# Optimization experiments

Measured on AMD Instinct MI355X. Metric: run time of the kernel, lower is better.

Reference implementation:

```python
import jax, jax.numpy as jnp
import numpy as np

WEIGHT_BITS = 8
INPUT_BITS = 8


def fake_quant(t, bits):
    """Per-tensor symmetric absmax fake quantization with straight-through estimator."""
    qmax = 2.0 ** (bits - 1) - 1.0  # e.g. 127 for 8 bits
    scale = jnp.maximum(jnp.max(jnp.abs(t)), 1e-8) / qmax
    q = jnp.round(t / scale) * scale
    return t + jax.lax.stop_gradient(q - t)


def setup_inputs() -> dict:
    key = jax.random.key(0)
    k0, k1, k2, k3 = jax.random.split(key, 4)
    d, f, n = 4096, 11008, 4096
    s_in = 1.0 / np.sqrt(d)
    s_ff = 1.0 / np.sqrt(f)
    return {
        "x": jax.random.normal(k0, (n, d), jnp.float32),
        "w1": jax.random.normal(k1, (f, d), jnp.float32) * s_in,  # fc1: embed -> ffn
        "w3": jax.random.normal(k2, (f, d), jnp.float32) * s_in,  # fc3: gate proj
        "w2": jax.random.normal(k3, (d, f), jnp.float32) * s_ff,  # fc2: ffn -> embed
    }


def reference(x, w1, w3, w2):
    # quantized fc3 -> silu gate
    xq = fake_quant(x, INPUT_BITS)
    gate = jax.nn.silu(jnp.einsum('nd,fd->nf', xq, fake_quant(w3, WEIGHT_BITS)))
    # quantized fc1, multiplied by gate (GLU)
    h = jnp.einsum('nd,fd->nf', xq, fake_quant(w1, WEIGHT_BITS)) * gate
    # subln=False -> no ffn_layernorm; dropout=0 (eval)
    hq = fake_quant(h, INPUT_BITS)
    out = jnp.einsum('nf,df->nd', hq, fake_quant(w2, WEIGHT_BITS))
    return out
```

## Files before the change

kernel.cpp:

```cpp
#include <hip/hip_runtime.h>
#include <hip/hip_bf16.h>

typedef __attribute__((ext_vector_type(4))) int int4v;

#define MFMA_I8(a, b, c) __builtin_amdgcn_mfma_i32_16x16x64_i8((a), (b), (c), 0, 0, 0)
#define GLDS16(g, l)                                                                        \
  __builtin_amdgcn_global_load_lds((const __attribute__((address_space(1))) void*)(g),      \
                                   (__attribute__((address_space(3))) void*)(l), 16, 0, 0)
#define SBAR() __builtin_amdgcn_s_barrier()
#define SCHED0() __builtin_amdgcn_sched_barrier(0)

static constexpr int NTOK = 4096;
static constexpr int DDIM = 4096;
static constexpr int FDIM = 11008;


__device__ __forceinline__ float wave_max64(float m) {
#pragma unroll
  for (int o = 32; o > 0; o >>= 1) m = fmaxf(m, __shfl_xor(m, o));
  return m;
}

__global__ void zero_slots(unsigned* s) {
  if (threadIdx.x < 16) s[threadIdx.x] = 0u;
}

__device__ __forceinline__ void absmax_body(const float* __restrict__ p, int n4,
                                            unsigned* __restrict__ slot) {
  float m = 0.f;
  const int stride = gridDim.x * blockDim.x;
  for (int i = blockIdx.x * blockDim.x + threadIdx.x; i < n4; i += stride) {
    float4 v = reinterpret_cast<const float4*>(p)[i];
    m = fmaxf(fmaxf(fabsf(v.x), fabsf(v.y)), fmaxf(fmaxf(fabsf(v.z), fabsf(v.w)), m));
  }
  m = wave_max64(m);
  __shared__ float wm[4];
  const int lane = threadIdx.x & 63, w = threadIdx.x >> 6;
  if (lane == 0) wm[w] = m;
  __syncthreads();
  if (threadIdx.x == 0) {
    m = fmaxf(fmaxf(wm[0], wm[1]), fmaxf(wm[2], wm[3]));
    atomicMax(slot, __float_as_uint(m));
  }
}

__global__ void absmax4(const float* x, const float* w1, const float* w3, const float* w2,
                        unsigned* slots, int n4x, int n4w) {
  const int seg = blockIdx.y;
  const float* p = (seg == 0) ? x : (seg == 1) ? w1 : (seg == 2) ? w3 : w2;
  absmax_body(p, seg == 0 ? n4x : n4w, slots + seg);
}

__device__ __forceinline__ void quant_body(const float* __restrict__ in,
                                           unsigned* __restrict__ out, int n4,
                                           const unsigned* __restrict__ slot) {
  const float s = fmaxf(__uint_as_float(*slot), 1e-8f) / 127.0f;
  const int stride = gridDim.x * blockDim.x;
  for (int i = blockIdx.x * blockDim.x + threadIdx.x; i < n4; i += stride) {
    float4 v = reinterpret_cast<const float4*>(in)[i];
    const int q0 = (int)rintf(v.x / s), q1 = (int)rintf(v.y / s);
    const int q2 = (int)rintf(v.z / s), q3 = (int)rintf(v.w / s);
    out[i] = (unsigned)(q0 & 255) | ((unsigned)(q1 & 255) << 8) |
             ((unsigned)(q2 & 255) << 16) | ((unsigned)(q3 & 255) << 24);
  }
}

__global__ void quant4(const float* x, const float* w1, const float* w3, const float* w2,
                       unsigned* qx, unsigned* qw1, unsigned* qw3, unsigned* qw2,
                       const unsigned* slots, int n4x, int n4w) {
  const int seg = blockIdx.y;
  const float* p = (seg == 0) ? x : (seg == 1) ? w1 : (seg == 2) ? w3 : w2;
  unsigned* o = (seg == 0) ? qx : (seg == 1) ? qw1 : (seg == 2) ? qw3 : qw2;
  quant_body(p, o, seg == 0 ? n4x : n4w, slots + seg);
}

__global__ void quant_kernel(const float* __restrict__ in, unsigned* __restrict__ out,
                             int n4, const unsigned* __restrict__ slot) {
  quant_body(in, out, n4, slot);
}

__global__ __launch_bounds__(512, 2) void gemm_glu(
    const signed char* __restrict__ Aq, const signed char* __restrict__ B3q,
    const signed char* __restrict__ B1q, float* __restrict__ H,
    const unsigned* __restrict__ slots, unsigned* __restrict__ hslot) {
  constexpr int K = DDIM;
  __shared__ char lds[163840];

  const int t = threadIdx.x;
  const int l = t & 63;
  const int w = t >> 6;

  const int gx = gridDim.x, gy = gridDim.y;
  const int nwg = gx * gy;
  const int i0 = blockIdx.y * gx + blockIdx.x;
  const int cid = (i0 & 7) * (nwg >> 3) + (i0 >> 3);
  const int rowA0 = (cid % gy) << 7;
  const int colB0 = (cid / gy) << 8;

  const int rlA = t >> 3;
  const int glA = (t & 7) ^ (rlA & 7);
  const signed char* aP = Aq + (size_t)(rowA0 + rlA) * K + glA * 16;
  const size_t r64 = (size_t)64 * K;
  const int stW = w * 1024;

  const int rlB = l >> 3;
  const int glB = (l & 7) ^ rlB;
  const signed char* b3P = B3q + (size_t)(colB0 + w * 32 + rlB) * K + glB * 16;
  const signed char* b1P = B1q + (size_t)(colB0 + w * 32 + rlB) * K + glB * 16;
  const size_t r8 = (size_t)8 * K;
  const int bBase3 = 16384 + w * 4096;
  const int bBase1 = 49152 + w * 4096;

#define STAGE_A(KO, BUF)                            \
  do {                                              \
    GLDS16(aP + (KO), &lds[(BUF) + stW]);           \
    GLDS16(aP + r64 + (KO), &lds[(BUF) + 8192 + stW]); \
  } while (0)

#define STAGE_B(KO, BUF)                                           \
  do {                                                             \
    GLDS16(b3P + (KO), &lds[(BUF) + bBase3]);                      \
    GLDS16(b3P + r8 + (KO), &lds[(BUF) + bBase3 + 1024]);          \
    GLDS16(b3P + 2 * r8 + (KO), &lds[(BUF) + bBase3 + 2048]);      \
    GLDS16(b3P + 3 * r8 + (KO), &lds[(BUF) + bBase3 + 3072]);      \
    GLDS16(b1P + (KO), &lds[(BUF) + bBase1]);                      \
    GLDS16(b1P + r8 + (KO), &lds[(BUF) + bBase1 + 1024]);          \
    GLDS16(b1P + 2 * r8 + (KO), &lds[(BUF) + bBase1 + 2048]);      \
    GLDS16(b1P + 3 * r8 + (KO), &lds[(BUF) + bBase1 + 3072]);      \
  } while (0)

#define LDSF(BASE, R, G)                                                      \
  (*reinterpret_cast<const int4v*>(                                           \
      &lds[(BASE) + (R)*128 + (((G) ^ ((R)&7)) << 4)]))

  int4v acc3[8][2], acc1[8][2];
#pragma unroll
  for (int m = 0; m < 8; ++m)
#pragma unroll
    for (int n = 0; n < 2; ++n) {
      acc3[m][n] = (int4v){0, 0, 0, 0};
      acc1[m][n] = (int4v){0, 0, 0, 0};
    }

  const int NT = K >> 7;
  const int lr = l & 15;
  const int cr = l >> 4;

  STAGE_A(0, 0);
  STAGE_B(0, 0);

  for (int kt = 0; kt < NT; ++kt) {
    const int rb = (kt & 1) * 81920;
    const bool haveNext = (kt + 1 < NT);

    SCHED0();
    asm volatile("s_waitcnt vmcnt(8)" ::: "memory");
    SBAR();
    SCHED0();

    if (haveNext) {
      const size_t kO = (size_t)(kt + 1) * 128;
      STAGE_A(kO, rb ^ 81920);
      STAGE_B(kO, rb ^ 81920);
    }

    int4v a[8];
#pragma unroll
    for (int m = 0; m < 8; ++m) a[m] = LDSF(rb, m * 16 + lr, cr);

    if (haveNext) {
      asm volatile("s_waitcnt vmcnt(10)" ::: "memory");
    } else {
      asm volatile("s_waitcnt vmcnt(0)" ::: "memory");
    }
    SCHED0();

    int4v b3f[2][2], b1f[2][2];
#pragma unroll
    for (int n = 0; n < 2; ++n) {
      const int R = n * 16 + lr;
      b3f[0][n] = LDSF(rb + bBase3, R, cr);
      b3f[1][n] = LDSF(rb + bBase3, R, 4 + cr);
      b1f[0][n] = LDSF(rb + bBase1, R, cr);
      b1f[1][n] = LDSF(rb + bBase1, R, 4 + cr);
    }

    __builtin_amdgcn_s_setprio(1);
#pragma unroll
    for (int m = 0; m < 8; ++m)
#pragma unroll
      for (int n = 0; n < 2; ++n) {
        acc3[m][n] = MFMA_I8(a[m], b3f[0][n], acc3[m][n]);
        acc1[m][n] = MFMA_I8(a[m], b1f[0][n], acc1[m][n]);
      }
    __builtin_amdgcn_s_setprio(0);

#pragma unroll
    for (int m = 0; m < 8; ++m) a[m] = LDSF(rb, m * 16 + lr, 4 + cr);
    __builtin_amdgcn_s_setprio(1);
#pragma unroll
    for (int m = 0; m < 8; ++m)
#pragma unroll
      for (int n = 0; n < 2; ++n) {
        acc3[m][n] = MFMA_I8(a[m], b3f[1][n], acc3[m][n]);
        acc1[m][n] = MFMA_I8(a[m], b1f[1][n], acc1[m][n]);
      }
    __builtin_amdgcn_s_setprio(0);
  }

  const float sx = fmaxf(__uint_as_float(slots[0]), 1e-8f) / 127.0f;
  const float sw1 = fmaxf(__uint_as_float(slots[1]), 1e-8f) / 127.0f;
  const float sw3 = fmaxf(__uint_as_float(slots[2]), 1e-8f) / 127.0f;
  const float s3 = sx * sw3, s1 = sx * sw1;
  const int crow0 = rowA0 + ((l >> 4) << 2);
  const int ccol0 = colB0 + w * 32 + lr;
  float hmax = 0.f;
#pragma unroll
  for (int m = 0; m < 8; ++m)
#pragma unroll
    for (int n = 0; n < 2; ++n)
#pragma unroll
      for (int j = 0; j < 4; ++j) {
        const int row = crow0 + m * 16 + j;
        const int col = ccol0 + n * 16;
        const float g = (float)acc3[m][n][j] * s3;
        const float gate = g / (1.f + expf(-g));
        const float h = (float)acc1[m][n][j] * s1 * gate;
        H[(size_t)row * FDIM + col] = h;
        hmax = fmaxf(hmax, fabsf(h));
      }
  hmax = wave_max64(hmax);
  if (l == 0) atomicMax(hslot, __float_as_uint(hmax));
#undef STAGE_A
#undef STAGE_B
#undef LDSF
}

__global__ __launch_bounds__(512, 2) void gemm_down(
    const signed char* __restrict__ Aq, const signed char* __restrict__ Bq,
    float* __restrict__ C, const unsigned* __restrict__ slots, int sA, int sB,
    int K, int ldc) {
  __shared__ char lds[131072];

  const int t = threadIdx.x;
  const int l = t & 63;
  const int w = t >> 6;
  const int wm = w >> 2;
  const int wn = w & 3;

  const int gx = gridDim.x, gy = gridDim.y;
  const int nwg = gx * gy;
  const int i0 = blockIdx.y * gx + blockIdx.x;
  const int cid = (i0 & 7) * (nwg >> 3) + (i0 >> 3);
  const int rowA0 = (cid % gy) << 8;
  const int colB0 = (cid / gy) << 8;

  const int rl = t >> 3;
  const int gl = (t & 7) ^ (rl & 7);
  const signed char* aP = Aq + (size_t)(rowA0 + rl) * K + gl * 16;
  const signed char* bP = Bq + (size_t)(colB0 + rl) * K + gl * 16;
  const size_t r64 = (size_t)64 * K;
  const int stW = w * 1024;

#define STAGE8(KO, BASE)                                             \
  do {                                                               \
    GLDS16(aP + (KO), &lds[(BASE) + stW]);                           \
    GLDS16(aP + r64 + (KO), &lds[(BASE) + 8192 + stW]);              \
    GLDS16(aP + 2 * r64 + (KO), &lds[(BASE) + 16384 + stW]);         \
    GLDS16(aP + 3 * r64 + (KO), &lds[(BASE) + 24576 + stW]);         \
    GLDS16(bP + (KO), &lds[(BASE) + 32768 + stW]);                   \
    GLDS16(bP + r64 + (KO), &lds[(BASE) + 40960 + stW]);             \
    GLDS16(bP + 2 * r64 + (KO), &lds[(BASE) + 49152 + stW]);         \
    GLDS16(bP + 3 * r64 + (KO), &lds[(BASE) + 57344 + stW]);         \
  } while (0)

#define LDSF(BASE, ROW, G)                                                    \
  (*reinterpret_cast<const int4v*>(                                           \
      &lds[(BASE) + (ROW)*128 + (((G) ^ ((ROW)&7)) << 4)]))

  int4v acc[8][4];
#pragma unroll
  for (int m = 0; m < 8; ++m)
#pragma unroll
    for (int n = 0; n < 4; ++n) acc[m][n] = (int4v){0, 0, 0, 0};

  const int NT = K >> 7;
  const int arow = wm * 128 + (l & 15);
  const int brow = wn * 64 + (l & 15);
  const int cr = l >> 4;

  STAGE8(0, 0);

  for (int kt = 0; kt < NT; ++kt) {
    const int rb = (kt & 1) * 65536;
    SCHED0();
    asm volatile("s_waitcnt vmcnt(0)" ::: "memory");
    SBAR();
    SCHED0();

    if (kt + 1 < NT) STAGE8((size_t)(kt + 1) * 128, rb ^ 65536);

#pragma unroll
    for (int kk = 0; kk < 2; ++kk) {
      int4v a[8], b[4];
#pragma unroll
      for (int m = 0; m < 8; ++m) a[m] = LDSF(rb, arow + m * 16, kk * 4 + cr);
#pragma unroll
      for (int n = 0; n < 4; ++n) b[n] = LDSF(rb + 32768, brow + n * 16, kk * 4 + cr);
      __builtin_amdgcn_s_setprio(1);
#pragma unroll
      for (int m = 0; m < 8; ++m)
#pragma unroll
        for (int n = 0; n < 4; ++n) acc[m][n] = MFMA_I8(a[m], b[n], acc[m][n]);
      __builtin_amdgcn_s_setprio(0);
    }
  }

  const float sa = fmaxf(__uint_as_float(slots[sA]), 1e-8f) / 127.0f;
  const float sb2 = fmaxf(__uint_as_float(slots[sB]), 1e-8f) / 127.0f;
  const float s = sa * sb2;
  const int crow0 = rowA0 + wm * 128 + ((l >> 4) << 2);
  const int ccol0 = colB0 + wn * 64 + (l & 15);
#pragma unroll
  for (int m = 0; m < 8; ++m)
#pragma unroll
    for (int n = 0; n < 4; ++n)
#pragma unroll
      for (int j = 0; j < 4; ++j) {
        const int row = crow0 + m * 16 + j;
        const int col = ccol0 + n * 16;
        C[(size_t)row * ldc + col] = (float)acc[m][n][j] * s;
      }
#undef STAGE8
#undef LDSF
}


extern "C" void kernel_launch(void* const* d_in, const int* in_sizes, int n_in,
                              void* d_out, int out_size, void* d_ws, size_t ws_size,
                              hipStream_t stream) {
  const float* x = (const float*)d_in[0];
  const float* w1 = (const float*)d_in[1];
  const float* w3 = (const float*)d_in[2];
  const float* w2 = (const float*)d_in[3];
  float* out = (float*)d_out;
  char* ws = (char*)d_ws;

  unsigned* slots = (unsigned*)ws;
  size_t off = 256;
  signed char* qx = (signed char*)(ws + off);
  off += (size_t)NTOK * DDIM;
  signed char* qw3 = (signed char*)(ws + off);
  off += (size_t)FDIM * DDIM;
  signed char* qw1 = (signed char*)(ws + off);
  off += (size_t)FDIM * DDIM;
  signed char* qw2 = (signed char*)(ws + off);
  off += (size_t)FDIM * DDIM;
  float* H = (float*)(ws + off);
  off += (size_t)NTOK * FDIM * 4;
  signed char* qh = (signed char*)(ws + off);
  off += (size_t)NTOK * FDIM;

  const int n4x = NTOK * DDIM / 4;
  const int n4w = FDIM * DDIM / 4;
  const int n4h = NTOK * FDIM / 4;

  zero_slots<<<1, 64, 0, stream>>>(slots);
  absmax4<<<dim3(512, 4), 256, 0, stream>>>(x, w1, w3, w2, slots, n4x, n4w);
  quant4<<<dim3(512, 4), 256, 0, stream>>>(x, w1, w3, w2, (unsigned*)qx, (unsigned*)qw1,
                                           (unsigned*)qw3, (unsigned*)qw2, slots, n4x, n4w);

  const dim3 gGlu(FDIM / 256, NTOK / 128);
  gemm_glu<<<gGlu, 512, 0, stream>>>(qx, qw3, qw1, H, slots, slots + 4);
  quant_kernel<<<2048, 256, 0, stream>>>(H, (unsigned*)qh, n4h, slots + 4);
  const dim3 gDn(DDIM / 256, NTOK / 256);
  gemm_down<<<gDn, 512, 0, stream>>>(qh, qw2, out, slots, 4, 3, FDIM, DDIM);
}
```

Measured before the change: 893.0 us.

## Pre-swizzle GLU weights into MFMA fragment order and load B directly to registers

The quantization pass now writes w1 and w3 in a fragment-major layout that matches the MFMA B-operand order for each lane. The GLU GEMM loads those fragments straight from global memory into registers, double-buffered two k-tiles ahead, instead of staging B through LDS. Only A goes through LDS, so LDS use drops from 160KB to 32KB. In exchange, B loads are no longer shared across waves through LDS and rely on global/L2 bandwidth and latency hiding in registers. The quant launch grid is also enlarged.

Result: slower. 1.516 ms (+69.7%).

```diff
diff --git a/kernel.cpp b/kernel.cpp
--- a/kernel.cpp
+++ b/kernel.cpp
@@ -3,6 +3,8 @@
 
 typedef __attribute__((ext_vector_type(4))) int int4v;
 
+#define MFMA_I8(a, b, c) __builtin_amdgcn_mfma_i32_32x32x16_i8
+#undef MFMA_I8
 #define MFMA_I8(a, b, c) __builtin_amdgcn_mfma_i32_16x16x64_i8((a), (b), (c), 0, 0, 0)
 #define GLDS16(g, l)                                                                        \
   __builtin_amdgcn_global_load_lds((const __attribute__((address_space(1))) void*)(g),      \
@@ -65,13 +67,43 @@
   }
 }
 
+__device__ __forceinline__ void quantW_frag_body(const float* __restrict__ in,
+                                                 int4v* __restrict__ out,
+                                                 const unsigned* __restrict__ slot) {
+  const float s = fmaxf(__uint_as_float(*slot), 1e-8f) / 127.0f;
+  const int total = FDIM * (DDIM / 16);
+  const int stride = gridDim.x * blockDim.x;
+  for (int u = blockIdx.x * blockDim.x + threadIdx.x; u < total; u += stride) {
+    const int block = u >> 8;
+    const int sidx = u & 255;
+    const int fi = sidx >> 6;
+    const int l = sidx & 63;
+    const int p = block >> 5;
+    const int kt = block & 31;
+    const int f = p * 32 + (fi & 1) * 16 + (l & 15);
+    const int k0 = kt * 128 + (fi >> 1) * 64 + (l >> 4) * 16;
+    const float4* src = reinterpret_cast<const float4*>(in + (size_t)f * DDIM + k0);
+    unsigned r[4];
+#pragma unroll
+    for (int j = 0; j < 4; ++j) {
+      float4 v = src[j];
+      const int q0 = (int)rintf(v.x / s), q1 = (int)rintf(v.y / s);
+      const int q2 = (int)rintf(v.z / s), q3 = (int)rintf(v.w / s);
+      r[j] = (unsigned)(q0 & 255) | ((unsigned)(q1 & 255) << 8) |
+             ((unsigned)(q2 & 255) << 16) | ((unsigned)(q3 & 255) << 24);
+    }
+    out[u] = (int4v){(int)r[0], (int)r[1], (int)r[2], (int)r[3]};
+  }
+}
+
 __global__ void quant4(const float* x, const float* w1, const float* w3, const float* w2,
                        unsigned* qx, unsigned* qw1, unsigned* qw3, unsigned* qw2,
                        const unsigned* slots, int n4x, int n4w) {
   const int seg = blockIdx.y;
-  const float* p = (seg == 0) ? x : (seg == 1) ? w1 : (seg == 2) ? w3 : w2;
-  unsigned* o = (seg == 0) ? qx : (seg == 1) ? qw1 : (seg == 2) ? qw3 : qw2;
-  quant_body(p, o, seg == 0 ? n4x : n4w, slots + seg);
+  if (seg == 0) quant_body(x, qx, n4x, slots + 0);
+  else if (seg == 1) quantW_frag_body(w1, (int4v*)qw1, slots + 1);
+  else if (seg == 2) quantW_frag_body(w3, (int4v*)qw3, slots + 2);
+  else quant_body(w2, qw2, n4w, slots + 3);
 }
 
 __global__ void quant_kernel(const float* __restrict__ in, unsigned* __restrict__ out,
@@ -80,11 +112,12 @@
 }
 
 __global__ __launch_bounds__(512, 2) void gemm_glu(
-    const signed char* __restrict__ Aq, const signed char* __restrict__ B3q,
-    const signed char* __restrict__ B1q, float* __restrict__ H,
+    const signed char* __restrict__ Aq, const signed char* __restrict__ B3f,
+    const signed char* __restrict__ B1f, float* __restrict__ H,
     const unsigned* __restrict__ slots, unsigned* __restrict__ hslot) {
   constexpr int K = DDIM;
-  __shared__ char lds[163840];
+  constexpr int NT = K >> 7;
+  __shared__ char lds[32768];
 
   const int t = threadIdx.x;
   const int l = t & 63;
@@ -103,30 +136,29 @@
   const size_t r64 = (size_t)64 * K;
   const int stW = w * 1024;
 
-  const int rlB = l >> 3;
-  const int glB = (l & 7) ^ rlB;
-  const signed char* b3P = B3q + (size_t)(colB0 + w * 32 + rlB) * K + glB * 16;
-  const signed char* b1P = B1q + (size_t)(colB0 + w * 32 + rlB) * K + glB * 16;
-  const size_t r8 = (size_t)8 * K;
-  const int bBase3 = 16384 + w * 4096;
-  const int bBase1 = 49152 + w * 4096;
-
-#define STAGE_A(KO, BUF)                            \
-  do {                                              \
-    GLDS16(aP + (KO), &lds[(BUF) + stW]);           \
-    GLDS16(aP + r64 + (KO), &lds[(BUF) + 8192 + stW]); \
+  const int p0 = (colB0 >> 5) + w;
+  const signed char* w3b = B3f + (size_t)p0 * 32 * 4096 + l * 16;
+  const signed char* w1b = B1f + (size_t)p0 * 32 * 4096 + l * 16;
+
+#define STAGE_A(KT, BUF)                                  \
+  do {                                                    \
+    const size_t kO_ = (size_t)(KT) * 128;                \
+    GLDS16(aP + kO_, &lds[(BUF) + stW]);                  \
+    GLDS16(aP + r64 + kO_, &lds[(BUF) + 8192 + stW]);     \
   } while (0)
 
-#define STAGE_B(KO, BUF)                                           \
-  do {                                                             \
-    GLDS16(b3P + (KO), &lds[(BUF) + bBase3]);                      \
-    GLDS16(b3P + r8 + (KO), &lds[(BUF) + bBase3 + 1024]);          \
-    GLDS16(b3P + 2 * r8 + (KO), &lds[(BUF) + bBase3 + 2048]);      \
-    GLDS16(b3P + 3 * r8 + (KO), &lds[(BUF) + bBase3 + 3072]);      \
-    GLDS16(b1P + (KO), &lds[(BUF) + bBase1]);                      \
-    GLDS16(b1P + r8 + (KO), &lds[(BUF) + bBase1 + 1024]);          \
-    GLDS16(b1P + 2 * r8 + (KO), &lds[(BUF) + bBase1 + 2048]);      \
-    GLDS16(b1P + 3 * r8 + (KO), &lds[(BUF) + bBase1 + 3072]);      \
+#define LOADB(KT, B3A, B1A)                                      \
+  do {                                                           \
+    const signed char* p3_ = w3b + (size_t)(KT)*4096;            \
+    const signed char* p1_ = w1b + (size_t)(KT)*4096;            \
+    B3A[0][0] = *(const int4v*)(p3_);                            \
+    B3A[0][1] = *(const int4v*)(p3_ + 1024);                     \
+    B3A[1][0] = *(const int4v*)(p3_ + 2048);                     \
+    B3A[1][1] = *(const int4v*)(p3_ + 3072);                     \
+    B1A[0][0] = *(const int4v*)(p1_);                            \
+    B1A[0][1] = *(const int4v*)(p1_ + 1024);                     \
+    B1A[1][0] = *(const int4v*)(p1_ + 2048);                     \
+    B1A[1][1] = *(const int4v*)(p1_ + 3072);                     \
   } while (0)
 
 #define LDSF(BASE, R, G)                                                      \
@@ -142,70 +174,54 @@
       acc1[m][n] = (int4v){0, 0, 0, 0};
     }
 
-  const int NT = K >> 7;
   const int lr = l & 15;
   const int cr = l >> 4;
 
+  int4v bc3[2][2], bc1[2][2], bn3[2][2], bn1[2][2];
+
   STAGE_A(0, 0);
-  STAGE_B(0, 0);
-
-  for (int kt = 0; kt < NT; ++kt) {
-    const int rb = (kt & 1) * 81920;
-    const bool haveNext = (kt + 1 < NT);
-
-    SCHED0();
-    asm volatile("s_waitcnt vmcnt(8)" ::: "memory");
-    SBAR();
-    SCHED0();
-
-    if (haveNext) {
-      const size_t kO = (size_t)(kt + 1) * 128;
-      STAGE_A(kO, rb ^ 81920);
-      STAGE_B(kO, rb ^ 81920);
-    }
-
-    int4v a[8];
-#pragma unroll
-    for (int m = 0; m < 8; ++m) a[m] = LDSF(rb, m * 16 + lr, cr);
-
-    if (haveNext) {
-      asm volatile("s_waitcnt vmcnt(10)" ::: "memory");
-    } else {
-      asm volatile("s_waitcnt vmcnt(0)" ::: "memory");
-    }
-    SCHED0();
-
-    int4v b3f[2][2], b1f[2][2];
-#pragma unroll
-    for (int n = 0; n < 2; ++n) {
-      const int R = n * 16 + lr;
-      b3f[0][n] = LDSF(rb + bBase3, R, cr);
-      b3f[1][n] = LDSF(rb + bBase3, R, 4 + cr);
-      b1f[0][n] = LDSF(rb + bBase1, R, cr);
-      b1f[1][n] = LDSF(rb + bBase1, R, 4 + cr);
-    }
-
-    __builtin_amdgcn_s_setprio(1);
-#pragma unroll
-    for (int m = 0; m < 8; ++m)
-#pragma unroll
-      for (int n = 0; n < 2; ++n) {
-        acc3[m][n] = MFMA_I8(a[m], b3f[0][n], acc3[m][n]);
-        acc1[m][n] = MFMA_I8(a[m], b1f[0][n], acc1[m][n]);
-      }
-    __builtin_amdgcn_s_setprio(0);
-
-#pragma unroll
-    for (int m = 0; m < 8; ++m) a[m] = LDSF(rb, m * 16 + lr, 4 + cr);
-    __builtin_amdgcn_s_setprio(1);
-#pragma unroll
-    for (int m = 0; m < 8; ++m)
-#pragma unroll
-      for (int n = 0; n < 2; ++n) {
-        acc3[m][n] = MFMA_I8(a[m], b3f[1][n], acc3[m][n]);
-        acc1[m][n] = MFMA_I8(a[m], b1f[1][n], acc1[m][n]);
-      }
-    __builtin_amdgcn_s_setprio(0);
+  LOADB(0, bc3, bc1);
+  LOADB(1, bn3, bn1);
+
+#define TILE(KT, C3, C1)                                                       \
+  do {                                                                         \
+    const int rb_ = ((KT)&1) * 16384;                                          \
+    SCHED0();                                                                  \
+    if ((KT) + 1 < NT) {                                                       \
+      asm volatile("s_waitcnt vmcnt(8)" ::: "memory");                         \
+    } else {                                                                   \
+      asm volatile("s_waitcnt vmcnt(0)" ::: "memory");                         \
+    }                                                                          \
+    SBAR();                                                                    \
+    SCHED0();                                                                  \
+    if ((KT) + 1 < NT) STAGE_A((KT) + 1, rb_ ^ 16384);                         \
+    int4v a_[8];                                                               \
+    _Pragma("unroll") for (int m = 0; m < 8; ++m)                              \
+        a_[m] = LDSF(rb_, m * 16 + lr, cr);                                    \
+    __builtin_amdgcn_s_setprio(1);                                             \
+    _Pragma("unroll") for (int m = 0; m < 8; ++m) {                            \
+      acc3[m][0] = MFMA_I8(a_[m], C3[0][0], acc3[m][0]);                       \
+      acc3[m][1] = MFMA_I8(a_[m], C3[0][1], acc3[m][1]);                       \
+      acc1[m][0] = MFMA_I8(a_[m], C1[0][0], acc1[m][0]);                       \
+      acc1[m][1] = MFMA_I8(a_[m], C1[0][1], acc1[m][1]);                       \
+    }                                                                          \
+    __builtin_amdgcn_s_setprio(0);                                             \
+    _Pragma("unroll") for (int m = 0; m < 8; ++m)                              \
+        a_[m] = LDSF(rb_, m * 16 + lr, 4 + cr);                                \
+    __builtin_amdgcn_s_setprio(1);                                             \
+    _Pragma("unroll") for (int m = 0; m < 8; ++m) {                            \
+      acc3[m][0] = MFMA_I8(a_[m], C3[1][0], acc3[m][0]);                       \
+      acc3[m][1] = MFMA_I8(a_[m], C3[1][1], acc3[m][1]);                       \
+      acc1[m][0] = MFMA_I8(a_[m], C1[1][0], acc1[m][0]);                       \
+      acc1[m][1] = MFMA_I8(a_[m], C1[1][1], acc1[m][1]);                       \
+    }                                                                          \
+    __builtin_amdgcn_s_setprio(0);                                             \
+    if ((KT) + 2 < NT) LOADB((KT) + 2, C3, C1);                                \
+  } while (0)
+
+  for (int kt = 0; kt < NT; kt += 2) {
+    TILE(kt, bc3, bc1);
+    TILE(kt + 1, bn3, bn1);
   }
 
   const float sx = fmaxf(__uint_as_float(slots[0]), 1e-8f) / 127.0f;
@@ -232,8 +248,9 @@
   hmax = wave_max64(hmax);
   if (l == 0) atomicMax(hslot, __float_as_uint(hmax));
 #undef STAGE_A
-#undef STAGE_B
+#undef LOADB
 #undef LDSF
+#undef TILE
 }
 
 __global__ __launch_bounds__(512, 2) void gemm_down(
@@ -367,8 +384,8 @@
 
   zero_slots<<<1, 64, 0, stream>>>(slots);
   absmax4<<<dim3(512, 4), 256, 0, stream>>>(x, w1, w3, w2, slots, n4x, n4w);
-  quant4<<<dim3(512, 4), 256, 0, stream>>>(x, w1, w3, w2, (unsigned*)qx, (unsigned*)qw1,
-                                           (unsigned*)qw3, (unsigned*)qw2, slots, n4x, n4w);
+  quant4<<<dim3(2048, 4), 256, 0, stream>>>(x, w1, w3, w2, (unsigned*)qx, (unsigned*)qw1,
+                                            (unsigned*)qw3, (unsigned*)qw2, slots, n4x, n4w);
 
   const dim3 gGlu(FDIM / 256, NTOK / 128);
   gemm_glu<<<gGlu, 512, 0, stream>>>(qx, qw3, qw1, H, slots, slots + 4);
```
